# Kernel optimization log

Hardware: AMD Instinct MI355X
Metric: run time of the kernel (lower is better)

The kernel has to match this reference:

```python
import jax, jax.numpy as jnp
from jax import lax
import numpy as np

ALIGN = 6                 # AlignW: pad width up to a multiple of align_width=6
W_BITS = 5
A_BITS = 5
A_MASK = (1 << A_BITS) - 1  # direct_conv2d bit-packs activations: keep low A_bits
DN = ('NCHW', 'OIHW', 'NCHW')


def _align_w(a):
    pad = (-a.shape[-1]) % ALIGN
    if pad:
        a = jnp.pad(a, ((0, 0), (0, 0), (0, 0), (0, pad)))
    return a


def _conv_relu(a, w, b):
    # nn.Conv2d(kernel_size=3, padding=2) + ReLU
    y = lax.conv_general_dilated(a, w, (1, 1), [(2, 2), (2, 2)], dimension_numbers=DN)
    return jax.nn.relu(y + b[None, :, None, None])


def _dc_conv(a, w):
    # DC_layer: integer direct conv2d, W_bits-quantized weights, A_bits activations,
    # stride 1, no padding (valid).
    aq = jnp.bitwise_and(a, A_MASK)
    return lax.conv_general_dilated(aq, w, (1, 1), [(0, 0), (0, 0)], dimension_numbers=DN,
                                    preferred_element_type=jnp.int32)


def _maxpool2(a):
    if jnp.issubdtype(a.dtype, jnp.floating):
        init = np.float32(-np.inf)
    else:
        init = np.int32(np.iinfo(np.int32).min)
    return lax.reduce_window(a, init, lax.max, (1, 1, 2, 2), (1, 1, 2, 2), 'VALID')


def _forward(x, ws, bs, qs, fc_w, fc_b):
    a = x
    k = 0
    for n in (2, 2, 3):          # float VGG blocks: [64,64,M, 128,128,M, 256,256,256,M]
        for _ in range(n):
            a = _conv_relu(_align_w(a), ws[k], bs[k])
            k += 1
        a = _maxpool2(a)
    # dequant stub is identity; x.int() truncates toward zero (a >= 0 after ReLU)
    xi = lax.stop_gradient(a).astype(jnp.int32)
    k = 0
    for n in (3, 3):             # DC blocks: [512,512,512,M, 512,512,512,M]
        for _ in range(n):
            xi = _dc_conv(_align_w(xi), qs[k])
            k += 1
        xi = _maxpool2(xi)
    # classifier: AdaptiveAvgPool2d((1,1)) + Flatten + Linear(512, 1000)
    pooled = jnp.mean(xi.astype(jnp.float32), axis=(2, 3))
    return pooled @ fc_w.T + fc_b


def setup_inputs() -> dict:
    key = jax.random.key(0)
    ks = jax.random.split(key, 24)
    d = {}
    d['x'] = jax.random.uniform(ks[0], (16, 3, 224, 224), jnp.float32) * 8.0
    conv_cfg = [(3, 64), (64, 64), (64, 128), (128, 128), (128, 256), (256, 256), (256, 256)]
    for i, (ci, co) in enumerate(conv_cfg):
        d[f'w{i + 1}'] = jax.random.normal(ks[1 + i], (co, ci, 3, 3), jnp.float32) * 0.1
        d[f'b{i + 1}'] = jax.random.normal(ks[8 + i], (co,), jnp.float32) * 0.1
    dc_cfg = [(256, 512)] + [(512, 512)] * 5
    for i, (ci, co) in enumerate(dc_cfg):
        # torch.randint(0, 2**W_bits - 1, ...) -> values in [0, 2**W_bits - 2]
        d[f'q{i + 1}'] = jax.random.randint(ks[15 + i], (co, ci, 3, 3), 0, 2 ** W_BITS - 1, jnp.int32)
    d['fc_w'] = jax.random.normal(ks[21], (1000, 512), jnp.float32) * 0.02
    d['fc_b'] = jnp.zeros((1000,), jnp.float32)
    return d


def reference(x, w1, w2, w3, w4, w5, w6, w7,
              b1, b2, b3, b4, b5, b6, b7,
              q1, q2, q3, q4, q5, q6, fc_w, fc_b):
    ws = (w1, w2, w3, w4, w5, w6, w7)
    bs = (b1, b2, b3, b4, b5, b6, b7)
    qs = (q1, q2, q3, q4, q5, q6)
    return _forward(x, ws, bs, qs, fc_w, fc_b)
```

## Files before the change

### kernel.cpp

```cpp
#include <hip/hip_runtime.h>
#include <cstddef>


typedef float v2f __attribute__((ext_vector_type(2)));

static __device__ __forceinline__ int dot4(int a, int b, int c) {
#if __has_builtin(__builtin_amdgcn_sdot4)
    return __builtin_amdgcn_sdot4(a, b, c, false);
#else
    return c + (a & 255) * (b & 255)
             + ((a >> 8) & 255) * ((b >> 8) & 255)
             + ((a >> 16) & 255) * ((b >> 16) & 255)
             + ((a >> 24) & 255) * ((b >> 24) & 255);
#endif
}

struct Rw { v2f a0, a1, a2, b0, b1; };

static __device__ __forceinline__ Rw ldr(const float* __restrict__ p) {
    Rw r;
    const float4 x = *reinterpret_cast<const float4*>(p);
    const float2 y = *reinterpret_cast<const float2*>(p + 4);
    const float4 z = *reinterpret_cast<const float4*>(p + 1);
    r.a0 = v2f{x.x, x.y}; r.a1 = v2f{x.z, x.w}; r.a2 = v2f{y.x, y.y};
    r.b0 = v2f{z.x, z.y}; r.b1 = v2f{z.z, z.w};
    return r;
}

static __device__ __forceinline__ void ld6i(const int* __restrict__ p, int v[6]) {
    const int4 a = *reinterpret_cast<const int4*>(p);
    const int2 b = *reinterpret_cast<const int2*>(p + 4);
    v[0] = a.x; v[1] = a.y; v[2] = a.z; v[3] = a.w; v[4] = b.x; v[5] = b.y;
}

static __device__ __forceinline__ void fmac8(const Rw v[3],
                                             const float* __restrict__ wr,
                                             v2f acc[8][2])
{
#pragma unroll
    for (int kh = 0; kh < 3; ++kh) {
        const Rw r = v[kh];
#pragma unroll
        for (int c = 0; c < 8; ++c) {
            const float k0 = wr[c * 9 + kh * 3 + 0];
            const float k1 = wr[c * 9 + kh * 3 + 1];
            const float k2 = wr[c * 9 + kh * 3 + 2];
            const v2f k0p = {k0, k0}, k1p = {k1, k1}, k2p = {k2, k2};
            v2f a0 = acc[c][0];
            a0 = __builtin_elementwise_fma(r.a1, k2p, a0);
            a0 = __builtin_elementwise_fma(r.b0, k1p, a0);
            a0 = __builtin_elementwise_fma(r.a0, k0p, a0);
            acc[c][0] = a0;
            v2f a1 = acc[c][1];
            a1 = __builtin_elementwise_fma(r.a2, k2p, a1);
            a1 = __builtin_elementwise_fma(r.b1, k1p, a1);
            a1 = __builtin_elementwise_fma(r.a1, k0p, a1);
            acc[c][1] = a1;
        }
    }
}

static __device__ __forceinline__ void fmac4p(const Rw v[4],
                                              const float* __restrict__ wr,
                                              v2f acc[4][2][2])
{
#pragma unroll
    for (int r = 0; r < 2; ++r) {
#pragma unroll
        for (int kh = 0; kh < 3; ++kh) {
            const Rw rv = v[r + kh];
#pragma unroll
            for (int c = 0; c < 4; ++c) {
                const float k0 = wr[c * 9 + kh * 3 + 0];
                const float k1 = wr[c * 9 + kh * 3 + 1];
                const float k2 = wr[c * 9 + kh * 3 + 2];
                const v2f k0p = {k0, k0}, k1p = {k1, k1}, k2p = {k2, k2};
                v2f a0 = acc[c][r][0];
                a0 = __builtin_elementwise_fma(rv.a1, k2p, a0);
                a0 = __builtin_elementwise_fma(rv.b0, k1p, a0);
                a0 = __builtin_elementwise_fma(rv.a0, k0p, a0);
                acc[c][r][0] = a0;
                v2f a1 = acc[c][r][1];
                a1 = __builtin_elementwise_fma(rv.a2, k2p, a1);
                a1 = __builtin_elementwise_fma(rv.b1, k1p, a1);
                a1 = __builtin_elementwise_fma(rv.a1, k0p, a1);
                acc[c][r][1] = a1;
            }
        }
    }
}

static __device__ __forceinline__ void dotc8(const int v[3][6],
                                             const int* __restrict__ wr,
                                             int acc[8][4])
{
#pragma unroll
    for (int kh = 0; kh < 3; ++kh) {
#pragma unroll
        for (int c = 0; c < 8; ++c) {
            const int k0 = wr[c * 9 + kh * 3 + 0];
            const int k1 = wr[c * 9 + kh * 3 + 1];
            const int k2 = wr[c * 9 + kh * 3 + 2];
#pragma unroll
            for (int t = 0; t < 4; ++t)
                acc[c][t] = dot4(v[kh][t], k0,
                            dot4(v[kh][t + 1], k1,
                            dot4(v[kh][t + 2], k2, acc[c][t])));
        }
    }
}

template<int CIN,int PH,int PW,int OH,int OW,int OPW,bool BORDER>
__global__ __launch_bounds__(256) void convf_k(
    const float* __restrict__ in, int instr,
    const float* __restrict__ wfp, const float* __restrict__ bias,
    float* __restrict__ out, int outstr, int total)
{
    constexpr int WB  = (OW + 3) / 4;
    constexpr int OPH = BORDER ? OH + 4 : OH;
    constexpr int OPL = OPH * OPW;
    const int s = blockIdx.z * 256 + threadIdx.x;
    if (s >= total) return;
    const int wb = s % WB;
    const int h  = (s / WB) % OH;
    const int n  = s / (WB * OH);
    const int w0 = wb * 4;
    const int cob = blockIdx.x;
    const int co0 = cob * 8;

    const float* ip = in + (size_t)n * instr + (size_t)h * PW + w0;
    const float* wl = wfp + (size_t)cob * CIN * 72;

    v2f acc[8][2];
#pragma unroll
    for (int c = 0; c < 8; ++c) { acc[c][0] = (v2f)0.f; acc[c][1] = (v2f)0.f; }

#pragma unroll 2
    for (int ci = 0; ci < CIN; ++ci) {
        Rw v[3];
#pragma unroll
        for (int kh = 0; kh < 3; ++kh) v[kh] = ldr(ip + kh * PW);
        fmac8(v, wl + (size_t)ci * 72, acc);
        ip += PH * PW;
    }

    float* ob = out + (size_t)n * outstr;
    const int ph  = BORDER ? h + 2 : h;
    const int pwo = BORDER ? 2 : 0;
#pragma unroll
    for (int c = 0; c < 8; ++c) {
        float* plane = ob + (size_t)(co0 + c) * OPL;
        float* row = plane + (size_t)ph * OPW;
        const float b = bias[co0 + c];
        const float av[4] = {acc[c][0][0], acc[c][0][1], acc[c][1][0], acc[c][1][1]};
#pragma unroll
        for (int t = 0; t < 4; ++t)
            if (w0 + t < OW) { const float r = av[t] + b; row[pwo + w0 + t] = r > 0.f ? r : 0.f; }
        if (BORDER) {
            if (wb == 0) { row[0] = 0.f; row[1] = 0.f; }
            if (wb == WB - 1) { for (int pw = OW + 2; pw < OPW; ++pw) row[pw] = 0.f; }
            if (h == 0 || h == OH - 1) {
                float* r0 = plane + (h == 0 ? 0 : (size_t)(OH + 2) * OPW);
                for (int rr = 0; rr < 2; ++rr) {
                    float* br = r0 + (size_t)rr * OPW;
#pragma unroll
                    for (int t = 0; t < 4; ++t) if (w0 + t < OW) br[2 + w0 + t] = 0.f;
                    if (wb == 0) { br[0] = 0.f; br[1] = 0.f; }
                    if (wb == WB - 1) { for (int pw = OW + 2; pw < OPW; ++pw) br[pw] = 0.f; }
                }
            }
        }
    }
}

template<int CIN,int PH,int PW,int POH,int POW,int OPW,int OY,int OX,int MODE>
__global__ __launch_bounds__(256) void convfp_k(
    const float* __restrict__ in, int instr,
    const float* __restrict__ wfp, const float* __restrict__ bias,
    void* __restrict__ outv, int outstr, int total)
{
    constexpr int WBp = POW / 2;
    constexpr int OPH = POH + 2 * OY;
    constexpr int OPL = OPH * OPW;
    const int s = blockIdx.z * 256 + threadIdx.x;
    if (s >= total) return;
    const int pb = s % WBp;
    const int ph = (s / WBp) % POH;
    const int n  = s / (WBp * POH);
    const int cob = blockIdx.x;
    const int co0 = cob * 4;

    const float* ip = in + (size_t)n * instr + (size_t)(2 * ph) * PW + 4 * pb;
    const float* wl = wfp + (size_t)cob * CIN * 36;

    v2f acc[4][2][2];
#pragma unroll
    for (int c = 0; c < 4; ++c)
#pragma unroll
        for (int r = 0; r < 2; ++r) { acc[c][r][0] = (v2f)0.f; acc[c][r][1] = (v2f)0.f; }

#pragma unroll 2
    for (int ci = 0; ci < CIN; ++ci) {
        Rw v[4];
#pragma unroll
        for (int r = 0; r < 4; ++r) v[r] = ldr(ip + r * PW);
        fmac4p(v, wl + (size_t)ci * 36, acc);
        ip += PH * PW;
    }

    float p[4][2];
#pragma unroll
    for (int c = 0; c < 4; ++c) {
        const float b = bias[co0 + c];
        float r00 = acc[c][0][0][0] + b; r00 = r00 > 0.f ? r00 : 0.f;
        float r01 = acc[c][0][0][1] + b; r01 = r01 > 0.f ? r01 : 0.f;
        float r02 = acc[c][0][1][0] + b; r02 = r02 > 0.f ? r02 : 0.f;
        float r03 = acc[c][0][1][1] + b; r03 = r03 > 0.f ? r03 : 0.f;
        float r10 = acc[c][1][0][0] + b; r10 = r10 > 0.f ? r10 : 0.f;
        float r11 = acc[c][1][0][1] + b; r11 = r11 > 0.f ? r11 : 0.f;
        float r12 = acc[c][1][1][0] + b; r12 = r12 > 0.f ? r12 : 0.f;
        float r13 = acc[c][1][1][1] + b; r13 = r13 > 0.f ? r13 : 0.f;
        float p0 = r00; p0 = p0 > r01 ? p0 : r01; p0 = p0 > r10 ? p0 : r10; p0 = p0 > r11 ? p0 : r11;
        float p1 = r02; p1 = p1 > r03 ? p1 : r03; p1 = p1 > r12 ? p1 : r12; p1 = p1 > r13 ? p1 : r13;
        p[c][0] = p0; p[c][1] = p1;
    }

    if constexpr (MODE == 1) {
        int* base = (int*)outv + (size_t)n * outstr + (size_t)cob * OPL
                  + (size_t)(OY + ph) * OPW + OX + 2 * pb;
        base[0] = (((int)p[0][0]) & 31) | ((((int)p[1][0]) & 31) << 8)
                | ((((int)p[2][0]) & 31) << 16) | ((((int)p[3][0]) & 31) << 24);
        base[1] = (((int)p[0][1]) & 31) | ((((int)p[1][1]) & 31) << 8)
                | ((((int)p[2][1]) & 31) << 16) | ((((int)p[3][1]) & 31) << 24);
        if (pb == WBp - 1) {
            int* row = (int*)outv + (size_t)n * outstr + (size_t)cob * OPL
                     + (size_t)(OY + ph) * OPW;
            for (int pw = OX + POW; pw < OPW; ++pw) row[pw] = 0;
        }
    } else {
#pragma unroll
        for (int c = 0; c < 4; ++c) {
            float* plane = (float*)outv + (size_t)n * outstr + (size_t)(co0 + c) * OPL;
            float* row = plane + (size_t)(OY + ph) * OPW;
            row[OX + 2 * pb]     = p[c][0];
            row[OX + 2 * pb + 1] = p[c][1];
            if (OX > 0 && pb == 0) { row[0] = 0.f; row[1] = 0.f; }
            if (pb == WBp - 1) { for (int pw = OX + POW; pw < OPW; ++pw) row[pw] = 0.f; }
            if (OY > 0 && (ph == 0 || ph == POH - 1)) {
                float* r0 = plane + (ph == 0 ? 0 : (size_t)(OY + POH) * OPW);
                for (int rr = 0; rr < OY; ++rr) {
                    float* br = r0 + (size_t)rr * OPW;
                    br[OX + 2 * pb] = 0.f; br[OX + 2 * pb + 1] = 0.f;
                    if (pb == 0) { br[0] = 0.f; br[1] = 0.f; }
                    if (pb == WBp - 1) { for (int pw = OX + POW; pw < OPW; ++pw) br[pw] = 0.f; }
                }
            }
        }
    }
}

template<int CIN4,int PH,int PW,int OH,int OW,int OPW,bool PACKOUT>
__global__ __launch_bounds__(256) void convq_k(
    const int* __restrict__ in, int instr, const int* __restrict__ wqp,
    int* __restrict__ out, int outstr, int total)
{
    constexpr int WB  = (OW + 3) / 4;
    constexpr int OPL = OH * OPW;
    const int s = blockIdx.z * 256 + threadIdx.x;
    if (s >= total) return;
    const int wb = s % WB;
    const int h  = (s / WB) % OH;
    const int n  = s / (WB * OH);
    const int w0 = wb * 4;
    const int cob = blockIdx.x;
    const int co0 = cob * 8;

    const int* ip = in + (size_t)n * instr + (size_t)h * PW + w0;
    const int* wl = wqp + (size_t)cob * CIN4 * 72;

    int acc[8][4];
#pragma unroll
    for (int c = 0; c < 8; ++c)
#pragma unroll
        for (int t = 0; t < 4; ++t) acc[c][t] = 0;

    int vb[3][6], vn[3][6];
#pragma unroll
    for (int kh = 0; kh < 3; ++kh) ld6i(ip + kh * PW, vb[kh]);

    for (int ci = 0; ci < CIN4; ci += 2) {
        ip += PH * PW;
#pragma unroll
        for (int kh = 0; kh < 3; ++kh) ld6i(ip + kh * PW, vn[kh]);
        dotc8(vb, wl + (size_t)ci * 72, acc);
        ip += PH * PW;
#pragma unroll
        for (int kh = 0; kh < 3; ++kh) ld6i(ip + kh * PW, vb[kh]);
        dotc8(vn, wl + (size_t)(ci + 1) * 72, acc);
    }

    if (PACKOUT) {
        int* base = out + (size_t)n * outstr + (size_t)(cob * 2) * OPL + (size_t)h * OPW + w0;
#pragma unroll
        for (int t = 0; t < 4; ++t) {
            if (w0 + t < OW) {
                const int lo = (acc[0][t] & 31) | ((acc[1][t] & 31) << 8)
                             | ((acc[2][t] & 31) << 16) | ((acc[3][t] & 31) << 24);
                const int hi = (acc[4][t] & 31) | ((acc[5][t] & 31) << 8)
                             | ((acc[6][t] & 31) << 16) | ((acc[7][t] & 31) << 24);
                base[t] = lo;
                base[OPL + t] = hi;
            }
        }
        if (wb == WB - 1) {
            for (int pw = OW; pw < OPW; ++pw) { base[pw - w0] = 0; base[OPL + pw - w0] = 0; }
        }
    } else {
        int* ob = out + (size_t)n * outstr;
#pragma unroll
        for (int c = 0; c < 8; ++c) {
            int* row = ob + (size_t)(co0 + c) * OPL + (size_t)h * OPW;
#pragma unroll
            for (int t = 0; t < 4; ++t)
                if (w0 + t < OW) row[w0 + t] = acc[c][t];
            if (wb == WB - 1) { for (int pw = OW; pw < OPW; ++pw) row[pw] = 0; }
        }
    }
}

__global__ void pack_wf_k(const float* __restrict__ w, float* __restrict__ out,
                          int CIN, int TC, int total)
{
    const int i = blockIdx.x * 256 + threadIdx.x;
    if (i >= total) return;
    const int r = i % 9;
    const int c = (i / 9) % TC;
    const int t = i / (9 * TC);
    const int ci = t % CIN;
    const int cob = t / CIN;
    out[i] = w[(((size_t)cob * TC + c) * CIN + ci) * 9 + r];
}

__global__ void pack_wq_k(const int* __restrict__ q, int* __restrict__ out,
                          int CIN4, int total)
{
    const int i = blockIdx.x * 256 + threadIdx.x;
    if (i >= total) return;
    const int r = i % 9;
    const int c = (i / 9) % 8;
    const int t = i / 72;
    const int ci4 = t % CIN4;
    const int cob = t / CIN4;
    const int co = cob * 8 + c;
    const int* p = q + ((size_t)co * CIN4 * 4 + ci4 * 4) * 9 + r;
    out[i] = (p[0] & 255) | ((p[9] & 255) << 8) | ((p[18] & 255) << 16) | ((p[27] & 255) << 24);
}

template<int C4,int HI,int WI,int HO,int WO,int OPH,int OPW>
__global__ void poolpack_k(const int* __restrict__ in, int instr,
                           int* __restrict__ out, int outstr, int total)
{
    const int i = blockIdx.x * 256 + threadIdx.x;
    if (i >= total) return;
    int t = i;
    const int px = t % OPW; t /= OPW;
    const int py = t % OPH; t /= OPH;
    const int c4 = t % C4;  const int n = t / C4;
    int word = 0;
    if (py < HO && px < WO) {
#pragma unroll
        for (int j = 0; j < 4; ++j) {
            const int* p = in + (size_t)n * instr
                         + ((size_t)(c4 * 4 + j) * HI + 2 * py) * WI + 2 * px;
            int m = p[0];
            m = m > p[1] ? m : p[1];
            m = m > p[WI] ? m : p[WI];
            m = m > p[WI + 1] ? m : p[WI + 1];
            word |= (m & 31) << (8 * j);
        }
    }
    out[(size_t)n * outstr + ((size_t)c4 * OPH + py) * OPW + px] = word;
}

template<int C,int HI,int WI,int HO,int WO,int OPH,int OPW>
__global__ void pool_i_k(const int* __restrict__ in, int instr,
                         int* __restrict__ out, int outstr, int total)
{
    const int i = blockIdx.x * 256 + threadIdx.x;
    if (i >= total) return;
    constexpr int OPL = OPH * OPW;
    int t = i;
    const int px = t % OPW; t /= OPW;
    const int py = t % OPH; t /= OPH;
    const int c  = t % C;   const int n = t / C;
    int v = 0;
    if (py < HO && px < WO) {
        const int* p = in + (size_t)n * instr + ((size_t)c * HI + 2 * py) * WI + 2 * px;
        int m = p[0];
        m = m > p[1] ? m : p[1];
        m = m > p[WI] ? m : p[WI];
        m = m > p[WI + 1] ? m : p[WI + 1];
        v = m;
    }
    out[(size_t)n * outstr + (size_t)c * OPL + (size_t)py * OPW + px] = v;
}

__global__ void copyin_k(const float* __restrict__ x, float* __restrict__ dst,
                         int outstr, int total)
{
    const int i = blockIdx.x * 256 + threadIdx.x;
    if (i >= total) return;
    int t = i;
    const int pw = t % 232; t /= 232;
    const int ph = t % 228; t /= 228;
    const int c  = t % 3;   const int n = t / 3;
    float v = 0.f;
    const int y = ph - 2, xx = pw - 2;
    if ((unsigned)y < 224u && (unsigned)xx < 224u)
        v = x[(size_t)n * 150528 + ((size_t)c * 224 + y) * 224 + xx];
    dst[(size_t)n * outstr + ((size_t)c * 228 + ph) * 232 + pw] = v;
}

__global__ void pool_mean_k(const int* __restrict__ in, int instr,
                            float* __restrict__ out, int outstr, int total)
{
    const int i = blockIdx.x * 256 + threadIdx.x;
    if (i >= total) return;
    const int n = i / 512, c = i % 512;
    const int* p = in + (size_t)n * instr + (size_t)c * 33;
    int s = 0;
#pragma unroll
    for (int j = 0; j < 33; ++j) s += p[j];
    out[(size_t)n * outstr + c] = (float)s / 33.0f;
}

__global__ void fc_k(const float* __restrict__ pooled, const float* __restrict__ w,
                     const float* __restrict__ b, float* __restrict__ out,
                     int nb, int n0)
{
    const int i = blockIdx.x * 256 + threadIdx.x;
    if (i >= nb * 1000) return;
    const int co = i % 1000;
    const int n  = i / 1000;
    const float4* pv = (const float4*)(pooled + (size_t)n * 512);
    const float4* wr = (const float4*)(w + (size_t)co * 512);
    float s = b[co];
    for (int c = 0; c < 128; ++c) {
        const float4 a = pv[c], q = wr[c];
        s = fmaf(a.x, q.x, s); s = fmaf(a.y, q.y, s);
        s = fmaf(a.z, q.z, s); s = fmaf(a.w, q.w, s);
    }
    out[(size_t)(n0 + n) * 1000 + co] = s;
}

extern "C" void kernel_launch(void* const* d_in, const int* in_sizes, int n_in,
                              void* d_out, int out_size, void* d_ws, size_t ws_size,
                              hipStream_t stream)
{
    (void)n_in; (void)out_size;
    const float* x = (const float*)d_in[0];
    const float* W[7]; const float* Bv[7]; const int* Q[6];
    const bool inter = (in_sizes[2] == 64);
    for (int i = 0; i < 7; ++i) {
        if (inter) { W[i] = (const float*)d_in[1 + 2 * i]; Bv[i] = (const float*)d_in[2 + 2 * i]; }
        else       { W[i] = (const float*)d_in[1 + i];     Bv[i] = (const float*)d_in[8 + i];     }
    }
    for (int i = 0; i < 6; ++i) Q[i] = (const int*)d_in[15 + i];
    const float* fcw = (const float*)d_in[21];
    const float* fcb = (const float*)d_in[22];
    float* outp = (float*)d_out;

    static const int FCO[7]  = {64, 64, 128, 128, 256, 256, 256};
    static const int FCIN[7] = {3, 64, 64, 128, 128, 256, 256};
    static const int FTC[7]  = {8, 4, 8, 4, 8, 8, 4};
    static const int QCIN4[6] = {64, 128, 128, 128, 128, 128};
    size_t wfoff[7], wft = 0;
    for (int i = 0; i < 7; ++i) { wfoff[i] = wft; wft += (size_t)FCO[i] * FCIN[i] * 9; }
    size_t wqoff[6], wqt = 0;
    for (int i = 0; i < 6; ++i) { wqoff[i] = wqt; wqt += (size_t)512 * QCIN4[i] * 9 * 4; }
    const size_t WTOT = wft + wqt;

    float* wfb = (float*)d_ws;
    int*   wqb = (int*)((float*)d_ws + wft);
    for (int i = 0; i < 7; ++i) {
        const int total = FCO[i] * FCIN[i] * 9;
        pack_wf_k<<<(total + 255) / 256, 256, 0, stream>>>(W[i], wfb + wfoff[i], FCIN[i], FTC[i], total);
    }
    for (int i = 0; i < 6; ++i) {
        const int total = 512 * QCIN4[i] * 9;
        pack_wq_k<<<(total + 255) / 256, 256, 0, stream>>>(Q[i], wqb + wqoff[i], QCIN4[i], total);
    }

    const long long SZ_X0 = 158688,  SZ_F1 = 3532800, SZ_P1 = 936448;
    const long long SZ_F4 = 2027520, SZ_P2 = 580608,  SZ_F7 = 1264640;
    const long long SZ_F8 = 1440768, SZ_PK1 = 90112;
    const long long SZ_D1 = 168960,  SZ_D2 = 157696,  SZ_D3 = 532480;
    const long long SZ_PK4 = 39936,  SZ_D4 = 33792,   SZ_D5 = 27648;
    const long long SZ_D6 = 86016,   SZ_P5 = 16896;
    const long long DCH = SZ_D1 + SZ_D2 + SZ_D3 + SZ_PK4 + SZ_D4 + SZ_D5 + SZ_D6 + SZ_P5 + 512;

    float* AR = (float*)d_ws + WTOT;
    long long AE2 = ((long long)(ws_size / 4) - (long long)WTOT - 20480) & ~3LL;

    int nbB = 16;
    for (;; nbB >>= 1) {
        if (nbB == 1) break;
        const long long f = nbB;
        const long long low = (nbB == 16) ? 0 : SZ_P1 * 16;
        const bool ok = (SZ_P1 * 16 + SZ_F4 * f <= AE2)
                     && (low + SZ_P2 * f <= AE2 - SZ_F4 * f)
                     && (low + SZ_F8 * f <= AE2 - SZ_F7 * f)
                     && (low + SZ_F8 * f <= AE2 - SZ_PK1 * f)
                     && (low + DCH * f <= AE2 - SZ_PK1 * f);
        if (ok) break;
    }
    int cA = 16;
    while (cA > 1 && SZ_P1 * 16 + (SZ_X0 + SZ_F1) * cA > AE2) cA >>= 1;

    const long long lowb = (nbB == 16) ? 0 : SZ_P1 * 16;
    float* tP1 = AR;
    float* tX0 = AR + SZ_P1 * 16;
    float* tF1 = tX0 + SZ_X0 * cA;
    float* tF4 = AR + (AE2 - SZ_F4 * nbB);
    float* tP2 = AR + lowb;
    float* tF7 = AR + (AE2 - SZ_F7 * nbB);
    float* tF8 = AR + lowb;
    int*   tPK1 = (int*)(AR + (AE2 - SZ_PK1 * nbB));
    int*   tD1 = (int*)(AR + lowb);
    int*   tD2 = tD1 + SZ_D1 * nbB;
    int*   tD3 = tD2 + SZ_D2 * nbB;
    int*   tPK4 = tD3 + SZ_D3 * nbB;
    int*   tD4 = tPK4 + SZ_PK4 * nbB;
    int*   tD5 = tD4 + SZ_D4 * nbB;
    int*   tD6 = tD5 + SZ_D5 * nbB;
    int*   tP5 = tD6 + SZ_D6 * nbB;
    float* tPP = (float*)(tP5 + SZ_P5 * nbB);

    for (int a0 = 0; a0 < 16; a0 += cA) {
        const int nb = cA;
        {
            const int total = nb * 3 * 228 * 232;
            copyin_k<<<(total + 255) / 256, 256, 0, stream>>>(
                x + (size_t)a0 * 150528, tX0, (int)SZ_X0, total);
        }
        {
            const int total = nb * 226 * 58;
            dim3 g(8, 1, (total + 255) / 256);
            convf_k<3, 228, 232, 226, 230, 240, true><<<g, 256, 0, stream>>>(
                tX0, (int)SZ_X0, wfb + wfoff[0], Bv[0], tF1, (int)SZ_F1, total);
        }
        {
            const int total = nb * 114 * 59;
            dim3 g(16, 1, (total + 255) / 256);
            convfp_k<64, 230, 240, 114, 118, 124, 2, 2, 0><<<g, 256, 0, stream>>>(
                tF1, (int)SZ_F1, wfb + wfoff[1], Bv[1],
                tP1 + (size_t)a0 * SZ_P1, (int)SZ_P1, total);
        }
    }

    for (int b0 = 0; b0 < 16; b0 += nbB) {
        const int nb = nbB;
        {
            const int total = nb * 116 * 31;
            dim3 g(16, 1, (total + 255) / 256);
            convf_k<64, 118, 124, 116, 122, 132, true><<<g, 256, 0, stream>>>(
                tP1 + (size_t)b0 * SZ_P1, (int)SZ_P1, wfb + wfoff[2], Bv[2],
                tF4, (int)SZ_F4, total);
        }
        {
            const int total = nb * 59 * 32;
            dim3 g(32, 1, (total + 255) / 256);
            convfp_k<128, 120, 132, 59, 64, 72, 2, 2, 0><<<g, 256, 0, stream>>>(
                tF4, (int)SZ_F4, wfb + wfoff[3], Bv[3], tP2, (int)SZ_P2, total);
        }
        {
            const int total = nb * 61 * 17;
            dim3 g(32, 1, (total + 255) / 256);
            convf_k<128, 63, 72, 61, 68, 76, true><<<g, 256, 0, stream>>>(
                tP2, (int)SZ_P2, wfb + wfoff[4], Bv[4], tF7, (int)SZ_F7, total);
        }
        {
            const int total = nb * 63 * 19;
            dim3 g(32, 1, (total + 255) / 256);
            convf_k<256, 65, 76, 63, 74, 84, true><<<g, 256, 0, stream>>>(
                tF7, (int)SZ_F7, wfb + wfoff[5], Bv[5], tF8, (int)SZ_F8, total);
        }
        {
            const int total = nb * 32 * 20;
            dim3 g(64, 1, (total + 255) / 256);
            convfp_k<256, 67, 84, 32, 40, 44, 0, 0, 1><<<g, 256, 0, stream>>>(
                tF8, (int)SZ_F8, wfb + wfoff[6], Bv[6], (void*)tPK1, (int)SZ_PK1, total);
        }
        {
            const int total = nb * 30 * 10;
            dim3 g(64, 1, (total + 255) / 256);
            convq_k<64, 32, 44, 30, 40, 44, true><<<g, 256, 0, stream>>>(
                tPK1, (int)SZ_PK1, wqb + wqoff[0], tD1, (int)SZ_D1, total);
        }
        {
            const int total = nb * 28 * 10;
            dim3 g(64, 1, (total + 255) / 256);
            convq_k<128, 30, 44, 28, 40, 44, true><<<g, 256, 0, stream>>>(
                tD1, (int)SZ_D1, wqb + wqoff[1], tD2, (int)SZ_D2, total);
        }
        {
            const int total = nb * 26 * 10;
            dim3 g(64, 1, (total + 255) / 256);
            convq_k<128, 28, 44, 26, 40, 40, false><<<g, 256, 0, stream>>>(
                tD2, (int)SZ_D2, wqb + wqoff[2], tD3, (int)SZ_D3, total);
        }
        {
            const int total = nb * 128 * 13 * 24;
            poolpack_k<128, 26, 40, 13, 20, 13, 24><<<(total + 255) / 256, 256, 0, stream>>>(
                tD3, (int)SZ_D3, tPK4, (int)SZ_PK4, total);
        }
        {
            const int total = nb * 11 * 6;
            dim3 g(64, 1, (total + 255) / 256);
            convq_k<128, 13, 24, 11, 22, 24, true><<<g, 256, 0, stream>>>(
                tPK4, (int)SZ_PK4, wqb + wqoff[3], tD4, (int)SZ_D4, total);
        }
        {
            const int total = nb * 9 * 6;
            dim3 g(64, 1, (total + 255) / 256);
            convq_k<128, 11, 24, 9, 22, 24, true><<<g, 256, 0, stream>>>(
                tD4, (int)SZ_D4, wqb + wqoff[4], tD5, (int)SZ_D5, total);
        }
        {
            const int total = nb * 7 * 6;
            dim3 g(64, 1, (total + 255) / 256);
            convq_k<128, 9, 24, 7, 22, 24, false><<<g, 256, 0, stream>>>(
                tD5, (int)SZ_D5, wqb + wqoff[5], tD6, (int)SZ_D6, total);
        }
        {
            const int total = nb * 512 * 33;
            pool_i_k<512, 7, 24, 3, 11, 3, 11><<<(total + 255) / 256, 256, 0, stream>>>(
                tD6, (int)SZ_D6, tP5, (int)SZ_P5, total);
        }
        {
            const int total = nb * 512;
            pool_mean_k<<<(total + 255) / 256, 256, 0, stream>>>(
                tP5, (int)SZ_P5, tPP, 512, total);
        }
        {
            const int total = nb * 1000;
            fc_k<<<(total + 255) / 256, 256, 0, stream>>>(tPP, fcw, fcb, outp, nb, b0);
        }
    }
}
```

Before: 5.786 ms.

## Stage input tiles in LDS for middle float conv layers

Adds a convf_t kernel that loads a halo-padded tile of each input channel into shared memory. A 4x64 grid of threads then computes from LDS instead of making overlapping global loads. It replaces convf_k for float conv layers 3, 5 and 6, and the workspace reserve grows so tile over-reads past the last plane stay in bounds. The remaining convf_k loop drops to unroll 1. The risk is two __syncthreads per input channel, with little load work per barrier, which can stall the pipeline.

```diff
diff --git a/kernel.cpp b/kernel.cpp
--- a/kernel.cpp
+++ b/kernel.cpp
@@ -110,6 +110,103 @@
     }
 }
 
+template<int CIN,int PH,int PW,int OH,int OW,int OPW,int TWB,int TH,bool BORDER>
+__global__ __launch_bounds__(256) void convf_t(
+    const float* __restrict__ in, int instr,
+    const float* __restrict__ wfp, const float* __restrict__ bias,
+    float* __restrict__ out, int outstr)
+{
+    constexpr int WB   = (OW + 3) / 4;
+    constexpr int WT   = (OW + 4 * TWB - 1) / (4 * TWB);
+    constexpr int HT   = (OH + TH - 1) / TH;
+    constexpr int ROWD = (TWB + 2) * 4;
+    constexpr int RF4  = TWB + 1;
+    constexpr int SC   = (TH + 2) * RF4;
+    constexpr int OPH  = BORDER ? OH + 4 : OH;
+    constexpr int OPL  = OPH * OPW;
+    __shared__ float lw[(TH + 2) * ROWD];
+
+    const int cob = blockIdx.x;
+    const int co0 = cob * 8;
+    int tz = blockIdx.z;
+    const int wt = tz % WT; tz /= WT;
+    const int ht = tz % HT; const int n = tz / HT;
+    const int w0t = wt * TWB * 4;
+    const int h0  = ht * TH;
+    const int tw = threadIdx.x % TWB;
+    const int th = threadIdx.x / TWB;
+
+    const float* plane0 = in + (size_t)n * instr + (size_t)h0 * PW + w0t;
+    const float* wl = wfp + (size_t)cob * CIN * 72;
+
+    v2f acc[8][2];
+#pragma unroll
+    for (int c = 0; c < 8; ++c) { acc[c][0] = (v2f)0.f; acc[c][1] = (v2f)0.f; }
+
+    for (int ci = 0; ci < CIN; ++ci) {
+        __syncthreads();
+        {
+            const float4* sp = (const float4*)(plane0 + (size_t)ci * PH * PW);
+#pragma unroll
+            for (int i0 = 0; i0 < SC; i0 += 256) {
+                const int i = i0 + threadIdx.x;
+                if (i < SC) {
+                    const int r = i / RF4, c = i % RF4;
+                    *(float4*)&lw[r * ROWD + 4 * c] = sp[(size_t)r * (PW / 4) + c];
+                }
+            }
+        }
+        __syncthreads();
+        {
+            const float* r0 = lw + th * ROWD + 4 * tw;
+            Rw v[3];
+#pragma unroll
+            for (int kh = 0; kh < 3; ++kh) {
+                const float* rp = r0 + kh * ROWD;
+                v[kh].a0 = *(const v2f*)(rp);
+                v[kh].a1 = *(const v2f*)(rp + 2);
+                v[kh].a2 = *(const v2f*)(rp + 4);
+                v[kh].b0 = v2f{rp[1], rp[2]};
+                v[kh].b1 = v2f{rp[3], rp[4]};
+            }
+            fmac8(v, wl + (size_t)ci * 72, acc);
+        }
+    }
+
+    const int h  = h0 + th;
+    const int w0 = w0t + 4 * tw;
+    if (h < OH) {
+        float* ob = out + (size_t)n * outstr;
+        const int wb = w0 / 4;
+        const int ph  = BORDER ? h + 2 : h;
+        const int pwo = BORDER ? 2 : 0;
+#pragma unroll
+        for (int c = 0; c < 8; ++c) {
+            float* plane = ob + (size_t)(co0 + c) * OPL;
+            float* row = plane + (size_t)ph * OPW;
+            const float b = bias[co0 + c];
+            const float av[4] = {acc[c][0][0], acc[c][0][1], acc[c][1][0], acc[c][1][1]};
+#pragma unroll
+            for (int t = 0; t < 4; ++t)
+                if (w0 + t < OW) { const float r = av[t] + b; row[pwo + w0 + t] = r > 0.f ? r : 0.f; }
+            if (BORDER) {
+                if (wb == 0) { row[0] = 0.f; row[1] = 0.f; }
+                if (wb == WB - 1) { for (int pw = OW + 2; pw < OPW; ++pw) row[pw] = 0.f; }
+                if (h == 0 || h == OH - 1) {
+                    float* r0 = plane + (h == 0 ? 0 : (size_t)(OH + 2) * OPW);
+                    for (int rr = 0; rr < 2; ++rr) {
+                        float* br = r0 + (size_t)rr * OPW;
+#pragma unroll
+                        for (int t = 0; t < 4; ++t) if (w0 + t < OW) br[2 + w0 + t] = 0.f;
+                        if (wb == 0) { br[0] = 0.f; br[1] = 0.f; }
+                        if (wb == WB - 1) { for (int pw = OW + 2; pw < OPW; ++pw) br[pw] = 0.f; }
+                    }
+                }
+            }
+        }
+    }
+}
+
 template<int CIN,int PH,int PW,int OH,int OW,int OPW,bool BORDER>
 __global__ __launch_bounds__(256) void convf_k(
     const float* __restrict__ in, int instr,
@@ -135,7 +232,7 @@
 #pragma unroll
     for (int c = 0; c < 8; ++c) { acc[c][0] = (v2f)0.f; acc[c][1] = (v2f)0.f; }
 
-#pragma unroll 2
+#pragma unroll 1
     for (int ci = 0; ci < CIN; ++ci) {
         Rw v[3];
 #pragma unroll
@@ -500,7 +597,7 @@
     const long long DCH = SZ_D1 + SZ_D2 + SZ_D3 + SZ_PK4 + SZ_D4 + SZ_D5 + SZ_D6 + SZ_P5 + 512;
 
     float* AR = (float*)d_ws + WTOT;
-    long long AE2 = ((long long)(ws_size / 4) - (long long)WTOT - 20480) & ~3LL;
+    long long AE2 = ((long long)(ws_size / 4) - (long long)WTOT - 65536) & ~3LL;
 
     int nbB = 16;
     for (;; nbB >>= 1) {
@@ -561,11 +658,10 @@
     for (int b0 = 0; b0 < 16; b0 += nbB) {
         const int nb = nbB;
         {
-            const int total = nb * 116 * 31;
-            dim3 g(16, 1, (total + 255) / 256);
-            convf_k<64, 118, 124, 116, 122, 132, true><<<g, 256, 0, stream>>>(
+            dim3 g(16, 1, nb * 2 * 8);
+            convf_t<64, 118, 124, 116, 122, 132, 4, 64, true><<<g, 256, 0, stream>>>(
                 tP1 + (size_t)b0 * SZ_P1, (int)SZ_P1, wfb + wfoff[2], Bv[2],
-                tF4, (int)SZ_F4, total);
+                tF4, (int)SZ_F4);
         }
         {
             const int total = nb * 59 * 32;
@@ -574,16 +670,14 @@
                 tF4, (int)SZ_F4, wfb + wfoff[3], Bv[3], tP2, (int)SZ_P2, total);
         }
         {
-            const int total = nb * 61 * 17;
-            dim3 g(32, 1, (total + 255) / 256);
-            convf_k<128, 63, 72, 61, 68, 76, true><<<g, 256, 0, stream>>>(
-                tP2, (int)SZ_P2, wfb + wfoff[4], Bv[4], tF7, (int)SZ_F7, total);
-        }
-        {
-            const int total = nb * 63 * 19;
-            dim3 g(32, 1, (total + 255) / 256);
-            convf_k<256, 65, 76, 63, 74, 84, true><<<g, 256, 0, stream>>>(
-                tF7, (int)SZ_F7, wfb + wfoff[5], Bv[5], tF8, (int)SZ_F8, total);
+            dim3 g(32, 1, nb * 5);
+            convf_t<128, 63, 72, 61, 68, 76, 4, 64, true><<<g, 256, 0, stream>>>(
+                tP2, (int)SZ_P2, wfb + wfoff[4], Bv[4], tF7, (int)SZ_F7);
+        }
+        {
+            dim3 g(32, 1, nb * 5);
+            convf_t<256, 65, 76, 63, 74, 84, 4, 64, true><<<g, 256, 0, stream>>>(
+                tF7, (int)SZ_F7, wfb + wfoff[5], Bv[5], tF8, (int)SZ_F8);
         }
         {
             const int total = nb * 32 * 20;
```

Measured after the change: 6.015 ms. +4.0%, slower.
